# Kernel tuning notes

Measured on AMD Instinct MI355X. Metric: run time of the kernel, lower is better.

The kernel has to match this reference:

```python
import jax, jax.numpy as jnp
import numpy as np

N = 4096
N_RBF = 16
N_HIDDEN = 64
CUTOFF = 5.0
R_MIN = 0.5
BOX = 40.0  # box side so ~30 neighbors fall within cutoff
ETA = 0.5 * (CUTOFF - R_MIN) / N_RBF  # 0.140625, matches RadialBasisLayer


def setup_inputs() -> dict:
    key = jax.random.key(0)
    ks = jax.random.split(key, 4)
    positions = jax.random.uniform(ks[0], (N, 3), dtype=jnp.float32) * BOX
    centers = jnp.linspace(R_MIN, CUTOFF, N_RBF, dtype=jnp.float32)  # buffer
    s1 = 1.0 / np.sqrt(N_RBF)
    s2 = 1.0 / np.sqrt(N_HIDDEN)
    W1 = jax.random.normal(ks[1], (N_RBF, N_HIDDEN), dtype=jnp.float32) * s1
    b1 = jnp.zeros((N_HIDDEN,), dtype=jnp.float32)
    W2 = jax.random.normal(ks[2], (N_HIDDEN, N_HIDDEN), dtype=jnp.float32) * s2
    b2 = jnp.zeros((N_HIDDEN,), dtype=jnp.float32)
    W3 = jax.random.normal(ks[3], (N_HIDDEN, 1), dtype=jnp.float32) * s2
    b3 = jnp.zeros((1,), dtype=jnp.float32)
    return {"positions": positions, "centers": centers,
            "W1": W1, "b1": b1, "W2": W2, "b2": b2, "W3": W3, "b3": b3}


def _features(positions, centers):
    # pairwise distances (N, N), safe sqrt for zero diagonal
    diff = positions[None, :, :] - positions[:, None, :]
    sq = jnp.sum(diff * diff, axis=-1)
    pos = sq > 0.0
    dist = jnp.where(pos, jnp.sqrt(jnp.where(pos, sq, 1.0)), 0.0)
    mask = pos & (dist < CUTOFF)  # (N, N)
    # RBF expansion with cosine smooth cutoff (vectorized over all pairs)
    x = dist / CUTOFF
    smooth = jnp.where(x < 1.0, 0.5 * (1.0 + jnp.cos(jnp.pi * x)), 0.0)
    w = jnp.where(mask, smooth, 0.0)  # fold mask into smooth weight (N, N)
    g = jnp.exp(-((dist[:, :, None] - centers) ** 2) / (2.0 * ETA * ETA))  # (N, N, n_rbf)
    feats = jnp.einsum('ijk,ij->ik', g, w)  # neighbor segment-sum -> (N, n_rbf)
    return feats


def reference(positions, centers, W1, b1, W2, b2, W3, b3):
    feats = _features(positions, centers)
    h = jax.nn.silu(feats @ W1 + b1)
    h = jax.nn.silu(h @ W2 + b2)
    atomic_e = (h @ W3 + b3)[:, 0]  # (N,)
    return jnp.sum(atomic_e)
```

## Files before the change

### kernel.cpp

```cpp
#include <hip/hip_runtime.h>
#include <math.h>

#define NATOMS   4096
#define NRBF     16
#define NHID     64
#define CUTOFF2  25.0f
#define INV_2ETA2 25.283950617283951f
#define PI_OVER_CUTOFF 0.62831853071795865f
#define CAP      96

#define NC1      8
#define NCELLS   512
#define CELLCAP  32
#define INV_CELL 0.2f

#define WS_ENERGY_OFF 0
#define WS_CNT_OFF    4096
#define WS_CELLS_OFF  5120
#define WS_NEED_BYTES ((size_t)(WS_CELLS_OFF + NCELLS * CELLCAP * 4) * 4)


__global__ __launch_bounds__(1024) void bin1_kernel(
    const float* __restrict__ pos,
    int* __restrict__ cnt,
    float4* __restrict__ cells)
{
    __shared__ int lcnt[NCELLS + 1];
    const int tid = threadIdx.x;
    if (tid < NCELLS + 1) lcnt[tid] = 0;
    __syncthreads();

    const float4* src = (const float4*)pos;
    const float4 v0 = src[3 * tid + 0];
    const float4 v1 = src[3 * tid + 1];
    const float4 v2 = src[3 * tid + 2];
    const float xs[4] = {v0.x, v0.w, v1.z, v2.y};
    const float ys[4] = {v0.y, v1.x, v1.w, v2.z};
    const float zs[4] = {v0.z, v1.y, v2.x, v2.w};
#pragma unroll
    for (int u = 0; u < 4; ++u) {
        const int cx = min((int)(xs[u] * INV_CELL), NC1 - 1);
        const int cy = min((int)(ys[u] * INV_CELL), NC1 - 1);
        const int cz = min((int)(zs[u] * INV_CELL), NC1 - 1);
        const int c  = (cz * NC1 + cy) * NC1 + cx;
        const int slot = atomicAdd(&lcnt[c], 1);
        if (slot < CELLCAP)
            cells[c * CELLCAP + slot] = make_float4(xs[u], ys[u], zs[u], 0.0f);
    }
    __syncthreads();
    if (tid < NCELLS + 1) cnt[tid] = lcnt[tid];
}

__global__ __launch_bounds__(256) void short_range_cells_kernel(
    const float* __restrict__ pos,
    const float* __restrict__ centers,
    const int* __restrict__ cnt,
    const float4* __restrict__ cells,
    const float* __restrict__ W1, const float* __restrict__ b1,
    const float* __restrict__ W2, const float* __restrict__ b2,
    const float* __restrict__ W3,
    float* __restrict__ ws)
{
    __shared__ float sdist[4][CAP];
    __shared__ float s_h1[4][NHID];

    const int tid  = threadIdx.x;
    const int lane = tid & 63;
    const int wave = tid >> 6;
    const int i    = blockIdx.x * 4 + wave;

    const float xi = pos[3 * i + 0];
    const float yi = pos[3 * i + 1];
    const float zi = pos[3 * i + 2];
    const int cxi = min((int)(xi * INV_CELL), NC1 - 1);
    const int cyi = min((int)(yi * INV_CELL), NC1 - 1);
    const int czi = min((int)(zi * INV_CELL), NC1 - 1);

    int nc = NCELLS;
    if (lane < 27) {
        const int cx = cxi + (lane % 3) - 1;
        const int cy = cyi + ((lane / 3) % 3) - 1;
        const int cz = czi + (lane / 9) - 1;
        if ((unsigned)cx < (unsigned)NC1 && (unsigned)cy < (unsigned)NC1 &&
            (unsigned)cz < (unsigned)NC1)
            nc = (cz * NC1 + cy) * NC1 + cx;
    }
    const int mycnt = min(cnt[nc], CELLCAP);

    const int half = lane >> 5;
    const int idx  = lane & 31;
    int base = 0;
#pragma unroll
    for (int t = 0; t < 14; ++t) {
        const int cl = 2 * t + half;
        const int c  = __shfl(nc,    cl, 64);
        const int cn = __shfl(mycnt, cl, 64);
        float sq = 1e30f;
        bool pass = false;
        if (idx < cn) {
            const float4 p = cells[c * CELLCAP + idx];
            const float dx = p.x - xi;
            const float dy = p.y - yi;
            const float dz = p.z - zi;
            sq = dx * dx + dy * dy + dz * dz;
            pass = (sq > 0.0f) && (sq < CUTOFF2);
        }
        const unsigned long long m = __ballot(pass);
        if (pass) {
            const int slot = base + (int)__popcll(m & ((1ull << lane) - 1ull));
            if (slot < CAP) sdist[wave][slot] = sqrtf(sq);
        }
        base += (int)__popcll(m);
    }
    const int count = min(base, CAP);

    const int   kf   = lane & 15;
    const int   eoff = lane >> 4;
    const float ck   = centers[kf];
    float acc = 0.0f;
    for (int e0 = 0; e0 < count; e0 += 4) {
        const int e = e0 + eoff;
        if (e < count) {
            const float d = sdist[wave][e];
            const float w = 0.5f * (1.0f + __cosf(d * PI_OVER_CUTOFF));
            const float t = d - ck;
            acc += w * __expf(-(t * t) * INV_2ETA2);
        }
    }
    acc += __shfl_xor(acc, 16, 64);
    acc += __shfl_xor(acc, 32, 64);

    float h = b1[lane];
#pragma unroll
    for (int k = 0; k < NRBF; ++k)
        h += __shfl(acc, k, 64) * W1[k * NHID + lane];
    h = h / (1.0f + __expf(-h));
    s_h1[wave][lane] = h;
    float h2 = b2[lane];
#pragma unroll 8
    for (int m = 0; m < NHID; ++m) h2 += s_h1[wave][m] * W2[m * NHID + lane];
    h2 = h2 / (1.0f + __expf(-h2));
    float e = h2 * W3[lane];
#pragma unroll
    for (int off = 32; off > 0; off >>= 1) e += __shfl_xor(e, off, 64);
    if (lane == 0) ws[i] = e;
}

__global__ __launch_bounds__(256) void reduce4k_kernel(
    const float* __restrict__ ws, const float* __restrict__ b3,
    float* __restrict__ out)
{
    __shared__ float s_part[4];
    const int tid  = threadIdx.x;
    const int lane = tid & 63;
    const int wave = tid >> 6;

    const float4* v4 = (const float4*)ws;
    float s = 0.0f;
#pragma unroll
    for (int k = 0; k < 4; ++k) {
        const float4 v = v4[tid + 256 * k];
        s += v.x + v.y + v.z + v.w;
    }
#pragma unroll
    for (int off = 32; off > 0; off >>= 1) s += __shfl_xor(s, off, 64);
    if (lane == 0) s_part[wave] = s;
    __syncthreads();
    if (tid == 0)
        out[0] = s_part[0] + s_part[1] + s_part[2] + s_part[3]
               + (float)NATOMS * b3[0];
}


#define CHUNK 1024

__global__ __launch_bounds__(256) void short_range_fb_kernel(
    const float* __restrict__ pos,
    const float* __restrict__ centers,
    const float* __restrict__ W1, const float* __restrict__ b1,
    const float* __restrict__ W2, const float* __restrict__ b2,
    const float* __restrict__ W3,
    float* __restrict__ ws)
{
    __shared__ float spos[3 * CHUNK];
    __shared__ float sdist[4][CAP];
    __shared__ float s_h1[4][NHID];
    __shared__ float s_part[4];

    const int tid  = threadIdx.x;
    const int lane = tid & 63;
    const int wave = tid >> 6;
    const int i    = blockIdx.x * 4 + wave;

    float* sx = spos;
    float* sy = spos + CHUNK;
    float* sz = spos + 2 * CHUNK;

    const float xi = pos[3 * i + 0];
    const float yi = pos[3 * i + 1];
    const float zi = pos[3 * i + 2];

    int base = 0;
    for (int c = 0; c < 4; ++c) {
        {
            const float4* src = (const float4*)(pos + c * (3 * CHUNK));
            const float4 v0 = src[3 * tid + 0];
            const float4 v1 = src[3 * tid + 1];
            const float4 v2 = src[3 * tid + 2];
            *(float4*)&sx[4 * tid] = make_float4(v0.x, v0.w, v1.z, v2.y);
            *(float4*)&sy[4 * tid] = make_float4(v0.y, v1.x, v1.w, v2.z);
            *(float4*)&sz[4 * tid] = make_float4(v0.z, v1.y, v2.x, v2.w);
        }
        __syncthreads();
#pragma unroll
        for (int it = 0; it < 4; ++it) {
            const int a = it * 256 + lane * 4;
            const float4 vx = *(const float4*)&sx[a];
            const float4 vy = *(const float4*)&sy[a];
            const float4 vz = *(const float4*)&sz[a];
#pragma unroll
            for (int u = 0; u < 4; ++u) {
                const float dx = ((const float*)&vx)[u] - xi;
                const float dy = ((const float*)&vy)[u] - yi;
                const float dz = ((const float*)&vz)[u] - zi;
                const float sq = dx * dx + dy * dy + dz * dz;
                const bool pass = (sq > 0.0f) && (sq < CUTOFF2);
                const unsigned long long mask = __ballot(pass);
                if (pass) {
                    const int slot = base + (int)__popcll(mask & ((1ull << lane) - 1ull));
                    if (slot < CAP) sdist[wave][slot] = sqrtf(sq);
                }
                base += (int)__popcll(mask);
            }
        }
        __syncthreads();
    }
    const int count = min(base, CAP);

    const int   kf   = lane & 15;
    const int   eoff = lane >> 4;
    const float ck   = centers[kf];
    float acc = 0.0f;
    for (int e0 = 0; e0 < count; e0 += 4) {
        const int e = e0 + eoff;
        if (e < count) {
            const float d = sdist[wave][e];
            const float w = 0.5f * (1.0f + __cosf(d * PI_OVER_CUTOFF));
            const float t = d - ck;
            acc += w * __expf(-(t * t) * INV_2ETA2);
        }
    }
    acc += __shfl_xor(acc, 16, 64);
    acc += __shfl_xor(acc, 32, 64);

    float h = b1[lane];
#pragma unroll
    for (int k = 0; k < NRBF; ++k)
        h += __shfl(acc, k, 64) * W1[k * NHID + lane];
    h = h / (1.0f + __expf(-h));
    s_h1[wave][lane] = h;
    float h2 = b2[lane];
#pragma unroll 8
    for (int m = 0; m < NHID; ++m) h2 += s_h1[wave][m] * W2[m * NHID + lane];
    h2 = h2 / (1.0f + __expf(-h2));
    float e = h2 * W3[lane];
#pragma unroll
    for (int off = 32; off > 0; off >>= 1) e += __shfl_xor(e, off, 64);
    if (lane == 0) s_part[wave] = e;
    __syncthreads();
    if (tid == 0)
        ws[blockIdx.x] = s_part[0] + s_part[1] + s_part[2] + s_part[3];
}

__global__ __launch_bounds__(256) void reduce_fb_kernel(
    const float* __restrict__ ws, const float* __restrict__ b3,
    float* __restrict__ out)
{
    __shared__ float s_part[4];
    const int tid  = threadIdx.x;
    const int lane = tid & 63;
    const int wave = tid >> 6;

    const float4 v = ((const float4*)ws)[tid];
    float s = v.x + v.y + v.z + v.w;
#pragma unroll
    for (int off = 32; off > 0; off >>= 1) s += __shfl_xor(s, off, 64);
    if (lane == 0) s_part[wave] = s;
    __syncthreads();
    if (tid == 0)
        out[0] = s_part[0] + s_part[1] + s_part[2] + s_part[3]
               + (float)NATOMS * b3[0];
}


extern "C" void kernel_launch(void* const* d_in, const int* in_sizes, int n_in,
                              void* d_out, int out_size, void* d_ws, size_t ws_size,
                              hipStream_t stream) {
    const float* pos     = (const float*)d_in[0];
    const float* centers = (const float*)d_in[1];
    const float* W1      = (const float*)d_in[2];
    const float* b1      = (const float*)d_in[3];
    const float* W2      = (const float*)d_in[4];
    const float* b2      = (const float*)d_in[5];
    const float* W3      = (const float*)d_in[6];
    const float* b3      = (const float*)d_in[7];
    float* out = (float*)d_out;
    float* ws  = (float*)d_ws;

    if (ws_size >= WS_NEED_BYTES) {
        int*    cnt   = (int*)(ws + WS_CNT_OFF);
        float4* cells = (float4*)(ws + WS_CELLS_OFF);
        hipLaunchKernelGGL(bin1_kernel, dim3(1), dim3(1024), 0, stream,
                           pos, cnt, cells);
        hipLaunchKernelGGL(short_range_cells_kernel, dim3(NATOMS / 4), dim3(256), 0, stream,
                           pos, centers, cnt, cells, W1, b1, W2, b2, W3,
                           ws + WS_ENERGY_OFF);
        hipLaunchKernelGGL(reduce4k_kernel, dim3(1), dim3(256), 0, stream,
                           ws + WS_ENERGY_OFF, b3, out);
    } else {
        hipLaunchKernelGGL(short_range_fb_kernel, dim3(NATOMS / 4), dim3(256), 0, stream,
                           pos, centers, W1, b1, W2, b2, W3, ws);
        hipLaunchKernelGGL(reduce_fb_kernel, dim3(1), dim3(256), 0, stream,
                           ws, b3, out);
    }
}
```

Before: 81.47 us.

## Fuse cell binning into per-block candidate gathering, drop separate bin kernel

Removes the single-block binning kernel and the global cell list. Each 4-atom block now marks its 27 neighbor cells in a shared bitmask, scans all 4096 positions, and appends the matching ones to per-wave shared candidate lists that are then distance-filtered. This saves one launch and the serialized single-block binning stage. In exchange, every one of the 1024 blocks reads all positions and performs shared atomics, which adds redundant work and makes the larger shared-memory footprint a possible occupancy limit.

```diff
diff --git a/kernel.cpp b/kernel.cpp
--- a/kernel.cpp
+++ b/kernel.cpp
@@ -8,61 +8,27 @@
 #define INV_2ETA2 25.283950617283951f
 #define PI_OVER_CUTOFF 0.62831853071795865f
 #define CAP      96
+#define CAP2     384
 
 #define NC1      8
 #define NCELLS   512
-#define CELLCAP  32
 #define INV_CELL 0.2f
 
-#define WS_ENERGY_OFF 0
-#define WS_CNT_OFF    4096
-#define WS_CELLS_OFF  5120
-#define WS_NEED_BYTES ((size_t)(WS_CELLS_OFF + NCELLS * CELLCAP * 4) * 4)
-
-
-__global__ __launch_bounds__(1024) void bin1_kernel(
-    const float* __restrict__ pos,
-    int* __restrict__ cnt,
-    float4* __restrict__ cells)
-{
-    __shared__ int lcnt[NCELLS + 1];
-    const int tid = threadIdx.x;
-    if (tid < NCELLS + 1) lcnt[tid] = 0;
-    __syncthreads();
-
-    const float4* src = (const float4*)pos;
-    const float4 v0 = src[3 * tid + 0];
-    const float4 v1 = src[3 * tid + 1];
-    const float4 v2 = src[3 * tid + 2];
-    const float xs[4] = {v0.x, v0.w, v1.z, v2.y};
-    const float ys[4] = {v0.y, v1.x, v1.w, v2.z};
-    const float zs[4] = {v0.z, v1.y, v2.x, v2.w};
-#pragma unroll
-    for (int u = 0; u < 4; ++u) {
-        const int cx = min((int)(xs[u] * INV_CELL), NC1 - 1);
-        const int cy = min((int)(ys[u] * INV_CELL), NC1 - 1);
-        const int cz = min((int)(zs[u] * INV_CELL), NC1 - 1);
-        const int c  = (cz * NC1 + cy) * NC1 + cx;
-        const int slot = atomicAdd(&lcnt[c], 1);
-        if (slot < CELLCAP)
-            cells[c * CELLCAP + slot] = make_float4(xs[u], ys[u], zs[u], 0.0f);
-    }
-    __syncthreads();
-    if (tid < NCELLS + 1) cnt[tid] = lcnt[tid];
-}
-
-__global__ __launch_bounds__(256) void short_range_cells_kernel(
+#define WS_NEED_BYTES ((size_t)(NATOMS) * 4)
+
+__global__ __launch_bounds__(256) void short_range_fused_kernel(
     const float* __restrict__ pos,
     const float* __restrict__ centers,
-    const int* __restrict__ cnt,
-    const float4* __restrict__ cells,
     const float* __restrict__ W1, const float* __restrict__ b1,
     const float* __restrict__ W2, const float* __restrict__ b2,
     const float* __restrict__ W3,
     float* __restrict__ ws)
 {
-    __shared__ float sdist[4][CAP];
-    __shared__ float s_h1[4][NHID];
+    __shared__ unsigned int nm32[NCELLS];
+    __shared__ int    ccount[4];
+    __shared__ float4 scand[4][CAP2];
+    __shared__ float  sdist[4][CAP];
+    __shared__ float  s_h1[4][NHID];
 
     const int tid  = threadIdx.x;
     const int lane = tid & 63;
@@ -76,29 +42,59 @@
     const int cyi = min((int)(yi * INV_CELL), NC1 - 1);
     const int czi = min((int)(zi * INV_CELL), NC1 - 1);
 
-    int nc = NCELLS;
+    nm32[tid]       = 0u;
+    nm32[tid + 256] = 0u;
+    if (tid < 4) ccount[tid] = 0;
+    __syncthreads();
+
     if (lane < 27) {
         const int cx = cxi + (lane % 3) - 1;
         const int cy = cyi + ((lane / 3) % 3) - 1;
         const int cz = czi + (lane / 9) - 1;
         if ((unsigned)cx < (unsigned)NC1 && (unsigned)cy < (unsigned)NC1 &&
             (unsigned)cz < (unsigned)NC1)
-            nc = (cz * NC1 + cy) * NC1 + cx;
-    }
-    const int mycnt = min(cnt[nc], CELLCAP);
-
-    const int half = lane >> 5;
-    const int idx  = lane & 31;
+            atomicOr(&nm32[(cz * NC1 + cy) * NC1 + cx], 1u << wave);
+    }
+    __syncthreads();
+
+    {
+        const float4* src = (const float4*)pos;
+#pragma unroll
+        for (int g = 0; g < 4; ++g) {
+            const float4 v0 = src[12 * tid + 3 * g + 0];
+            const float4 v1 = src[12 * tid + 3 * g + 1];
+            const float4 v2 = src[12 * tid + 3 * g + 2];
+            const float xs[4] = {v0.x, v0.w, v1.z, v2.y};
+            const float ys[4] = {v0.y, v1.x, v1.w, v2.z};
+            const float zs[4] = {v0.z, v1.y, v2.x, v2.w};
+#pragma unroll
+            for (int u = 0; u < 4; ++u) {
+                const int cx = min((int)(xs[u] * INV_CELL), NC1 - 1);
+                const int cy = min((int)(ys[u] * INV_CELL), NC1 - 1);
+                const int cz = min((int)(zs[u] * INV_CELL), NC1 - 1);
+                const unsigned m = nm32[(cz * NC1 + cy) * NC1 + cx];
+#pragma unroll
+                for (int w = 0; w < 4; ++w) {
+                    if ((m >> w) & 1u) {
+                        const int slot = atomicAdd(&ccount[w], 1);
+                        if (slot < CAP2)
+                            scand[w][slot] =
+                                make_float4(xs[u], ys[u], zs[u], 0.0f);
+                    }
+                }
+            }
+        }
+    }
+    __syncthreads();
+
+    const int cnt = min(ccount[wave], CAP2);
     int base = 0;
-#pragma unroll
-    for (int t = 0; t < 14; ++t) {
-        const int cl = 2 * t + half;
-        const int c  = __shfl(nc,    cl, 64);
-        const int cn = __shfl(mycnt, cl, 64);
+    for (int j0 = 0; j0 < cnt; j0 += 64) {
+        const int j = j0 + lane;
         float sq = 1e30f;
         bool pass = false;
-        if (idx < cn) {
-            const float4 p = cells[c * CELLCAP + idx];
+        if (j < cnt) {
+            const float4 p = scand[wave][j];
             const float dx = p.x - xi;
             const float dy = p.y - yi;
             const float dz = p.z - zi;
@@ -308,15 +304,10 @@
     float* ws  = (float*)d_ws;
 
     if (ws_size >= WS_NEED_BYTES) {
-        int*    cnt   = (int*)(ws + WS_CNT_OFF);
-        float4* cells = (float4*)(ws + WS_CELLS_OFF);
-        hipLaunchKernelGGL(bin1_kernel, dim3(1), dim3(1024), 0, stream,
-                           pos, cnt, cells);
-        hipLaunchKernelGGL(short_range_cells_kernel, dim3(NATOMS / 4), dim3(256), 0, stream,
-                           pos, centers, cnt, cells, W1, b1, W2, b2, W3,
-                           ws + WS_ENERGY_OFF);
+        hipLaunchKernelGGL(short_range_fused_kernel, dim3(NATOMS / 4), dim3(256), 0, stream,
+                           pos, centers, W1, b1, W2, b2, W3, ws);
         hipLaunchKernelGGL(reduce4k_kernel, dim3(1), dim3(256), 0, stream,
-                           ws + WS_ENERGY_OFF, b3, out);
+                           ws, b3, out);
     } else {
         hipLaunchKernelGGL(short_range_fb_kernel, dim3(NATOMS / 4), dim3(256), 0, stream,
                            pos, centers, W1, b1, W2, b2, W3, ws);
```

Result: slower. 86.01 us (+5.6%).
